# Optimization experiments

Hardware: AMD Instinct MI355X
Metric: run time of the kernel (lower is better)

## Reference

```python
import jax, jax.numpy as jnp
import numpy as np

# ---- fixed structural constants from the module source ----
BODY_PARTS = [[1, 2, 3], [4, 5, 6], [0, 7, 8, 9, 10], [11, 12, 13], [14, 15, 16]]
PART_EDGES = [[0, 2], [1, 2], [2, 3], [2, 4]]
N_JOINTS, N_PARTS = 17, 5
K_CHEB = 3  # ChebConv K=2 -> K+1 = 3 polynomial terms


def _pool_scatter_mats():
    # P[p, j] = 1/len(part_p) for j in part_p  (AdaptiveAvgPool1d(1) == mean)
    P = np.zeros((N_PARTS, N_JOINTS), np.float32)
    # S[j, p] = 1 if joint j belongs to part p (broadcast scatter)
    S = np.zeros((N_JOINTS, N_PARTS), np.float32)
    for p, idxs in enumerate(BODY_PARTS):
        for j in idxs:
            P[p, j] = 1.0 / len(idxs)
            S[j, p] = 1.0
    return jnp.asarray(P), jnp.asarray(S)


def _part_adj():
    # adj_mx_from_edges: symmetrize, add self loops, row-normalize
    A = np.zeros((N_PARTS, N_PARTS), np.float32)
    for i, j in PART_EDGES:
        A[i, j] = 1.0
    A = A + A.T  # edges are one-directional and disjoint -> symmetrize
    A = A + np.eye(N_PARTS, dtype=np.float32)
    A = A / A.sum(axis=1, keepdims=True)  # row-normalize
    return jnp.asarray(A)


def _cheb_basis(adj):
    # get_laplacian(normalize=True): L = I - D^{-1/2} A D^{-1/2}
    d_isqrt = jnp.sum(adj, axis=-1) ** (-0.5)
    L = jnp.eye(N_PARTS, dtype=adj.dtype) - (d_isqrt[:, None] * adj) * d_isqrt[None, :]
    I = jnp.eye(N_PARTS, dtype=adj.dtype)
    T2 = 2.0 * (L @ L) - I  # Chebyshev recurrence, K=2
    return jnp.stack([I, L, T2], axis=0)  # [3, 5, 5]


def setup_inputs() -> dict:
    key = jax.random.key(0)
    k1, k2 = jax.random.split(key)
    B, D = 8192, 512
    x = jax.random.normal(k1, (B, N_JOINTS, D), dtype=jnp.float32)
    # xavier-normal-like init for ChebConv weight [K+1, 1, in_c, out_c]
    scale = (2.0 / (D + D)) ** 0.5
    weight = jax.random.normal(k2, (K_CHEB, 1, D, D), dtype=jnp.float32) * scale
    bias = jnp.zeros((1, 1, D), dtype=jnp.float32)
    return {"x": x, "weight": weight, "bias": bias}


def reference(x, weight, bias):
    # x: [B, 17, D]; weight: [3, 1, D, D]; bias: [1, 1, D]
    P, S = _pool_scatter_mats()
    cheb = _cheb_basis(_part_adj())            # [3, 5, 5]
    part_feats = jnp.einsum('pj,bjd->bpd', P, x)              # part-wise mean pool
    prop = jnp.einsum('knm,bmd->kbnd', cheb, part_feats)      # Cheb propagation
    part_out = jnp.einsum('kbnd,kde->bne', prop, weight[:, 0]) + bias[0]  # [B, 5, D]
    return jnp.einsum('jp,bpd->bjd', S, part_out)             # broadcast to 17 joints
```

## Files before the change

### kernel.cpp

```cpp
#include <hip/hip_runtime.h>
#include <hip/hip_bf16.h>
#include <stdint.h>
#include <stddef.h>

typedef __attribute__((ext_vector_type(8))) short short8;
typedef __attribute__((ext_vector_type(4))) float f32x4;
typedef __attribute__((ext_vector_type(4))) unsigned int u32x4;

#define DIM   512
#define NJ    17
#define NPART 5
#define NB    8192
#define KDIM  1536
#define QROWS (NB*NPART)
#define ROWB  (KDIM*2)

struct Cheb { float c[3][5][5]; };

__device__ __forceinline__ void gload_lds16(const void* g, void* l) {
  __builtin_amdgcn_global_load_lds((__attribute__((address_space(1))) void*)(g),
                                   (__attribute__((address_space(3))) void*)(l),
                                   16, 0, 0);
}

__global__ __launch_bounds__(256) void pool_cheb_kernel(
    const float* __restrict__ x, __hip_bfloat16* __restrict__ Q, Cheb cb) {
  int gid = blockIdx.x * 256 + threadIdx.x;
  int b  = gid >> 7;
  int c4 = gid & 127;
  const float* xb = x + (size_t)b * (NJ * DIM) + (c4 << 2);

  f32x4 pf[5];
#pragma unroll
  for (int p = 0; p < 5; ++p) pf[p] = (f32x4){0.f, 0.f, 0.f, 0.f};

  constexpr int jpart[NJ] = {2,0,0,0,1,1,1,2,2,2,2,3,3,3,4,4,4};
#pragma unroll
  for (int j = 0; j < NJ; ++j) {
    f32x4 a = __builtin_nontemporal_load(
        reinterpret_cast<const f32x4*>(xb + j * DIM));
    pf[jpart[j]] += a;
  }
  constexpr float scl[5] = {1.f/3.f, 1.f/3.f, 0.2f, 1.f/3.f, 1.f/3.f};
#pragma unroll
  for (int p = 0; p < 5; ++p) pf[p] *= scl[p];

  char* qb = reinterpret_cast<char*>(Q);
  int cj = c4 >> 1;
#pragma unroll
  for (int k = 0; k < 3; ++k) {
#pragma unroll
    for (int n = 0; n < 5; ++n) {
      int row = b * 5 + n;
      f32x4 s = cb.c[k][n][0] * pf[0] + cb.c[k][n][1] * pf[1] +
                cb.c[k][n][2] * pf[2] + cb.c[k][n][3] * pf[3] +
                cb.c[k][n][4] * pf[4];
      alignas(8) __hip_bfloat16 o[4];
#pragma unroll
      for (int i = 0; i < 4; ++i) o[i] = __float2bfloat16(s[i]);
      int swc = (cj & 7) ^ (row & 7);
      size_t off = (size_t)row * ROWB + (size_t)(k * 8 + (cj >> 3)) * 128 +
                   (size_t)swc * 16 + (size_t)(c4 & 1) * 8;
      *reinterpret_cast<ushort4*>(qb + off) = *reinterpret_cast<const ushort4*>(o);
    }
  }
}

__global__ __launch_bounds__(256) void wt_kernel(
    const float* __restrict__ w, __hip_bfloat16* __restrict__ Wt) {
  int gid = blockIdx.x * 256 + threadIdx.x;
  int e = gid & 511;
  int chunk = gid >> 9;
  int kidx0 = chunk << 3;
  alignas(16) __hip_bfloat16 o[8];
#pragma unroll
  for (int i = 0; i < 8; ++i)
    o[i] = __float2bfloat16(w[(size_t)(kidx0 + i) * DIM + e]);
  int blk = kidx0 >> 6;
  int swc = ((kidx0 >> 3) & 7) ^ (e & 7);
  size_t off = (size_t)e * ROWB + (size_t)blk * 128 + (size_t)swc * 16;
  *reinterpret_cast<u32x4*>(reinterpret_cast<char*>(Wt) + off) =
      *reinterpret_cast<const u32x4*>(o);
}

__global__ __launch_bounds__(512, 2) void gemm_big_kernel(
    const __hip_bfloat16* __restrict__ Q, const __hip_bfloat16* __restrict__ Wt,
    const float* __restrict__ bias, float* __restrict__ out) {
  extern __shared__ __align__(16) char LDSbuf[];
  char* As0 = LDSbuf;
  char* As1 = LDSbuf + 40960;
  char* Bs0 = LDSbuf + 81920;
  char* Bs1 = LDSbuf + 114688;

  int tid  = threadIdx.x;
  int lane = tid & 63;
  int wave = tid >> 6;
  int wr = wave >> 1, wc = wave & 1;
  int m0 = blockIdx.y * 320;
  int n0 = blockIdx.x * 256;

  f32x4 acc[5][8] = {};

  const char* qb = reinterpret_cast<const char*>(Q);
  const char* wb = reinterpret_cast<const char*>(Wt);
  int sr8 = lane >> 3;
  int sc  = (lane & 7) * 16;

  const char* abase = qb + (size_t)(m0 + wave * 40 + sr8) * ROWB + sc;
  const char* bbase = wb + (size_t)(n0 + wave * 32 + sr8) * ROWB + sc;
  char* aldsw = (char*)0 + wave * 5120;
  char* bldsw = (char*)0 + wave * 4096;

  auto stage = [&](char* Abuf, char* Bbuf, int ks) {
#pragma unroll
    for (int i = 0; i < 5; ++i)
      gload_lds16(abase + (size_t)i * (8 * ROWB) + (size_t)ks * 128,
                  Abuf + (size_t)(aldsw - (char*)0) + i * 1024);
#pragma unroll
    for (int i = 0; i < 4; ++i)
      gload_lds16(bbase + (size_t)i * (8 * ROWB) + (size_t)ks * 128,
                  Bbuf + (size_t)(bldsw - (char*)0) + i * 1024);
  };

  auto compute = [&](const char* Abuf, const char* Bbuf) {
#pragma unroll
    for (int kk = 0; kk < 2; ++kk) {
      short8 af[5];
#pragma unroll
      for (int mi = 0; mi < 5; ++mi) {
        int r = wr * 80 + mi * 16 + (lane & 15);
        int c7 = (kk * 4 + (lane >> 4)) ^ (r & 7);
        af[mi] = *reinterpret_cast<const short8*>(Abuf + r * 128 + c7 * 16);
      }
#pragma unroll
      for (int h = 0; h < 2; ++h) {
        short8 bf[4];
#pragma unroll
        for (int nj = 0; nj < 4; ++nj) {
          int r = wc * 128 + (h * 4 + nj) * 16 + (lane & 15);
          int c7 = (kk * 4 + (lane >> 4)) ^ (r & 7);
          bf[nj] = *reinterpret_cast<const short8*>(Bbuf + r * 128 + c7 * 16);
        }
#pragma unroll
        for (int mi = 0; mi < 5; ++mi)
#pragma unroll
          for (int nj = 0; nj < 4; ++nj)
            acc[mi][h * 4 + nj] = __builtin_amdgcn_mfma_f32_16x16x32_bf16(
                af[mi], bf[nj], acc[mi][h * 4 + nj], 0, 0, 0);
      }
    }
  };

  stage(As0, Bs0, 0);
  __syncthreads();
  for (int ks = 0; ks < 22; ks += 2) {
    stage(As1, Bs1, ks + 1);
    compute(As0, Bs0);
    __syncthreads();
    stage(As0, Bs0, ks + 2);
    compute(As1, Bs1);
    __syncthreads();
  }
  stage(As1, Bs1, 23);
  compute(As0, Bs0);
  __syncthreads();
  compute(As1, Bs1);
  __syncthreads();

  float bs[8];
#pragma unroll
  for (int ni = 0; ni < 8; ++ni)
    bs[ni] = bias[n0 + wc * 128 + ni * 16 + (lane & 15)];

  char* eb = LDSbuf + wave * 8448;
  int halfsel = lane >> 5;
  int col4 = lane & 31;

#pragma unroll
  for (int mi = 0; mi < 5; ++mi) {
#pragma unroll
    for (int ni = 0; ni < 8; ++ni)
#pragma unroll
      for (int j = 0; j < 4; ++j) {
        int row = (lane >> 4) * 4 + j;
        *reinterpret_cast<float*>(
            eb + ((row * 132 + ni * 16 + (lane & 15)) << 2)) =
            acc[mi][ni][j] + bs[ni];
      }
#pragma unroll
    for (int rr = 0; rr < 8; ++rr) {
      int row = rr * 2 + halfsel;
      u32x4 v4 = *reinterpret_cast<const u32x4*>(
          eb + ((row * 132 + col4 * 4) << 2));
      int R = m0 + wr * 80 + mi * 16 + row;
      unsigned bb = (unsigned)R / 5u;
      int n = R - (int)bb * 5;
      unsigned mask = (n == 0) ? 0x0000Eu :
                      (n == 1) ? 0x00070u :
                      (n == 2) ? 0x00781u :
                      (n == 3) ? 0x03800u : 0x1C000u;
      float* op = out + (size_t)bb * (NJ * DIM) + (n0 + wc * 128 + col4 * 4);
      while (mask) {
        int jn = __builtin_ctz(mask);
        mask &= mask - 1;
        __builtin_nontemporal_store(v4, reinterpret_cast<u32x4*>(op + jn * DIM));
      }
    }
  }
}

__global__ __launch_bounds__(512) void gemm_scatter_kernel(
    const __hip_bfloat16* __restrict__ Q, const __hip_bfloat16* __restrict__ Wt,
    const float* __restrict__ bias, float* __restrict__ out) {
  __shared__ __align__(16) char LDSbuf[49152];
  char* As = LDSbuf;
  char* Bs = LDSbuf + 32768;

  int tid  = threadIdx.x;
  int lane = tid & 63;
  int wave = tid >> 6;
  int wr = wave >> 1, wc = wave & 1;
  int m0 = blockIdx.y * 256;
  int n0 = blockIdx.x * 128;

  f32x4 acc[4][4] = {};

  const char* qb = reinterpret_cast<const char*>(Q);
  const char* wb = reinterpret_cast<const char*>(Wt);
  int sr8 = lane >> 3;
  int sc  = (lane & 7) * 16;

  for (int ks = 0; ks < 24; ++ks) {
#pragma unroll
    for (int i = 0; i < 4; ++i) {
      int rbase = i * 64 + wave * 8;
      gload_lds16(qb + (size_t)(m0 + rbase + sr8) * ROWB + (size_t)ks * 128 + sc,
                  As + rbase * 128);
    }
#pragma unroll
    for (int i = 0; i < 2; ++i) {
      int rbase = i * 64 + wave * 8;
      gload_lds16(wb + (size_t)(n0 + rbase + sr8) * ROWB + (size_t)ks * 128 + sc,
                  Bs + rbase * 128);
    }
    __syncthreads();
#pragma unroll
    for (int kk = 0; kk < 2; ++kk) {
      short8 af[4], bfr[4];
#pragma unroll
      for (int mi = 0; mi < 4; ++mi) {
        int r = wr * 64 + mi * 16 + (lane & 15);
        int c7 = (kk * 4 + (lane >> 4)) ^ (r & 7);
        af[mi] = *reinterpret_cast<const short8*>(As + r * 128 + c7 * 16);
      }
#pragma unroll
      for (int ni = 0; ni < 4; ++ni) {
        int r = wc * 64 + ni * 16 + (lane & 15);
        int c7 = (kk * 4 + (lane >> 4)) ^ (r & 7);
        bfr[ni] = *reinterpret_cast<const short8*>(Bs + r * 128 + c7 * 16);
      }
#pragma unroll
      for (int mi = 0; mi < 4; ++mi)
#pragma unroll
        for (int ni = 0; ni < 4; ++ni)
          acc[mi][ni] = __builtin_amdgcn_mfma_f32_16x16x32_bf16(
              af[mi], bfr[ni], acc[mi][ni], 0, 0, 0);
    }
    __syncthreads();
  }

  int colbase = n0 + wc * 64 + (lane & 15);
  float bs[4];
#pragma unroll
  for (int ni = 0; ni < 4; ++ni) bs[ni] = bias[colbase + ni * 16];

  char* eb = LDSbuf + wave * 4352;
  int g4 = lane >> 4;
  int cc = lane & 15;

#pragma unroll
  for (int mi = 0; mi < 4; ++mi) {
#pragma unroll
    for (int ni = 0; ni < 4; ++ni)
#pragma unroll
      for (int j = 0; j < 4; ++j)
        *reinterpret_cast<float*>(
            eb + (((g4 * 4 + j) * 68 + ni * 16 + cc) << 2)) =
            acc[mi][ni][j] + bs[ni];

#pragma unroll
    for (int t = 0; t < 4; ++t) {
      u32x4 v4 = *reinterpret_cast<const u32x4*>(
          eb + ((((t * 4 + g4) * 68) + cc * 4) << 2));
      int R4 = m0 + wr * 64 + mi * 16 + t * 4 + g4;
      unsigned bb = (unsigned)R4 / 5u;
      int n = R4 - (int)bb * 5;
      unsigned mask = (n == 0) ? 0x0000Eu :
                      (n == 1) ? 0x00070u :
                      (n == 2) ? 0x00781u :
                      (n == 3) ? 0x03800u : 0x1C000u;
      float* op = out + (size_t)bb * (NJ * DIM) + (n0 + wc * 64 + cc * 4);
      while (mask) {
        int jn = __builtin_ctz(mask);
        mask &= mask - 1;
        __builtin_nontemporal_store(v4, reinterpret_cast<u32x4*>(op + jn * DIM));
      }
    }
  }
}

extern "C" void kernel_launch(void* const* d_in, const int* in_sizes, int n_in,
                              void* d_out, int out_size, void* d_ws, size_t ws_size,
                              hipStream_t stream) {
  const float* x    = (const float*)d_in[0];
  const float* w    = (const float*)d_in[1];
  const float* bias = (const float*)d_in[2];
  float* out = (float*)d_out;

  __hip_bfloat16* Q  = (__hip_bfloat16*)d_ws;
  __hip_bfloat16* Wt = (__hip_bfloat16*)((char*)d_ws + (size_t)QROWS * ROWB);

  Cheb cb;
  {
    double A[5][5] = {};
    const int e0[4] = {0, 1, 2, 2}, e1[4] = {2, 2, 3, 4};
    for (int t = 0; t < 4; ++t) { A[e0[t]][e1[t]] = 1.0; A[e1[t]][e0[t]] = 1.0; }
    for (int i = 0; i < 5; ++i) A[i][i] += 1.0;
    for (int i = 0; i < 5; ++i) {
      double rs = 0; for (int j = 0; j < 5; ++j) rs += A[i][j];
      for (int j = 0; j < 5; ++j) A[i][j] /= rs;
    }
    double L[5][5], T2[5][5];
    for (int i = 0; i < 5; ++i)
      for (int j = 0; j < 5; ++j) L[i][j] = (i == j ? 1.0 : 0.0) - A[i][j];
    for (int i = 0; i < 5; ++i)
      for (int j = 0; j < 5; ++j) {
        double s = 0; for (int m = 0; m < 5; ++m) s += L[i][m] * L[m][j];
        T2[i][j] = 2.0 * s - (i == j ? 1.0 : 0.0);
      }
    for (int i = 0; i < 5; ++i)
      for (int j = 0; j < 5; ++j) {
        cb.c[0][i][j] = (float)(i == j ? 1.0 : 0.0);
        cb.c[1][i][j] = (float)L[i][j];
        cb.c[2][i][j] = (float)T2[i][j];
      }
  }

  pool_cheb_kernel<<<(NB * 128) / 256, 256, 0, stream>>>(x, Q, cb);
  wt_kernel<<<(DIM * (KDIM / 8)) / 256, 256, 0, stream>>>(w, Wt);

  const int DYN_LDS = 147456;
  hipError_t e = hipFuncSetAttribute(
      reinterpret_cast<const void*>(gemm_big_kernel),
      hipFuncAttributeMaxDynamicSharedMemorySize, DYN_LDS);
  if (e == hipSuccess) {
    gemm_big_kernel<<<dim3(DIM / 256, QROWS / 320), 512, DYN_LDS, stream>>>(
        Q, Wt, bias, out);
  } else {
    gemm_scatter_kernel<<<dim3(DIM / 128, QROWS / 256), 512, 0, stream>>>(
        Q, Wt, bias, out);
  }
}
```

Measured before the change: 172.7 us.

## Fuse pooling/Chebyshev propagation into GEMM, staging A operand in LDS

Adds a fused kernel in which each 1024-thread block pools 32 batch items, applies the Chebyshev mixing and writes the bf16 A operand directly into LDS. It then runs the MFMA GEMM over the full 512 output columns and scatters the results to the 17 joints. This removes the global round trip of the Q intermediate and one kernel launch. The weight is re-laid out so that K tiles interleave with the pooling chunks. The cost is a single wave of work per block, with x loads serialized against compute behind syncthreads and no double buffering of B.

```diff
diff --git a/kernel.cpp b/kernel.cpp
--- a/kernel.cpp
+++ b/kernel.cpp
@@ -5,6 +5,7 @@
 
 typedef __attribute__((ext_vector_type(8))) short short8;
 typedef __attribute__((ext_vector_type(4))) float f32x4;
+typedef __attribute__((ext_vector_type(2))) float f32x2;
 typedef __attribute__((ext_vector_type(4))) unsigned int u32x4;
 
 #define DIM   512
@@ -23,6 +24,162 @@
                                    16, 0, 0);
 }
 
+__global__ __launch_bounds__(1024, 4) void fused_kernel(
+    const float* __restrict__ x, const __hip_bfloat16* __restrict__ Wt2,
+    const float* __restrict__ bias, float* __restrict__ out, Cheb cb) {
+  extern __shared__ __align__(16) char LDS[];
+  char* Aseg = LDS;
+  char* Bs   = LDS + 61440;
+
+  int tid  = threadIdx.x;
+  int lane = tid & 63;
+  int wave = tid >> 6;
+  int wr = wave >> 3;
+  int wc = wave & 7;
+  int b0    = blockIdx.x * 32;
+  int prow0 = blockIdx.x * 160;
+
+  f32x4 acc[5][4] = {};
+
+  int bl = tid >> 5;
+  int dd = tid & 31;
+  const float* xb = x + (size_t)(b0 + bl) * (NJ * DIM) + (dd << 1);
+  constexpr int jpart[NJ] = {2,0,0,0,1,1,1,2,2,2,2,3,3,3,4,4,4};
+  constexpr float scl[5] = {1.f/3.f, 1.f/3.f, 0.2f, 1.f/3.f, 1.f/3.f};
+
+  const char* wb = reinterpret_cast<const char*>(Wt2);
+
+  for (int db = 0; db < 8; ++db) {
+    f32x2 pf[5];
+#pragma unroll
+    for (int p = 0; p < 5; ++p) pf[p] = (f32x2){0.f, 0.f};
+    const float* xd = xb + db * 64;
+#pragma unroll
+    for (int j = 0; j < NJ; ++j) {
+      f32x2 a = __builtin_nontemporal_load(
+          reinterpret_cast<const f32x2*>(xd + j * DIM));
+      pf[jpart[j]] += a;
+    }
+#pragma unroll
+    for (int p = 0; p < 5; ++p) pf[p] *= scl[p];
+
+#pragma unroll
+    for (int k = 0; k < 3; ++k) {
+#pragma unroll
+      for (int n = 0; n < 5; ++n) {
+        int row = bl * 5 + n;
+        f32x2 s = cb.c[k][n][0] * pf[0] + cb.c[k][n][1] * pf[1] +
+                  cb.c[k][n][2] * pf[2] + cb.c[k][n][3] * pf[3] +
+                  cb.c[k][n][4] * pf[4];
+        alignas(4) __hip_bfloat16 o2[2];
+        o2[0] = __float2bfloat16(s[0]);
+        o2[1] = __float2bfloat16(s[1]);
+        *reinterpret_cast<unsigned int*>(
+            Aseg + k * 20480 + row * 128 +
+            (((dd >> 2) ^ (row & 7)) << 4) + ((dd & 3) << 2)) =
+            *reinterpret_cast<const unsigned int*>(o2);
+      }
+    }
+
+#pragma unroll
+    for (int k = 0; k < 3; ++k) {
+      int ks = db * 3 + k;
+#pragma unroll
+      for (int i = 0; i < 4; ++i) {
+        int rbase = i * 128 + wave * 8;
+        gload_lds16(wb + (size_t)(rbase + (lane >> 3)) * ROWB +
+                        (size_t)ks * 128 + (lane & 7) * 16,
+                    Bs + rbase * 128);
+      }
+      __syncthreads();
+
+      const char* Ab = Aseg + k * 20480;
+#pragma unroll
+      for (int kk = 0; kk < 2; ++kk) {
+        short8 af[5], bf[4];
+#pragma unroll
+        for (int mi = 0; mi < 5; ++mi) {
+          int r = wr * 80 + mi * 16 + (lane & 15);
+          int c7 = (kk * 4 + (lane >> 4)) ^ (r & 7);
+          af[mi] = *reinterpret_cast<const short8*>(Ab + r * 128 + c7 * 16);
+        }
+#pragma unroll
+        for (int nj = 0; nj < 4; ++nj) {
+          int r = wc * 64 + nj * 16 + (lane & 15);
+          int c7 = (kk * 4 + (lane >> 4)) ^ (r & 7);
+          bf[nj] = *reinterpret_cast<const short8*>(Bs + r * 128 + c7 * 16);
+        }
+#pragma unroll
+        for (int mi = 0; mi < 5; ++mi)
+#pragma unroll
+          for (int nj = 0; nj < 4; ++nj)
+            acc[mi][nj] = __builtin_amdgcn_mfma_f32_16x16x32_bf16(
+                af[mi], bf[nj], acc[mi][nj], 0, 0, 0);
+      }
+      __syncthreads();
+    }
+  }
+
+  float bs[4];
+#pragma unroll
+  for (int ni = 0; ni < 4; ++ni)
+    bs[ni] = bias[wc * 64 + ni * 16 + (lane & 15)];
+
+  char* eb = LDS + wave * 4352;
+  int g4 = lane >> 4;
+  int cc = lane & 15;
+
+#pragma unroll
+  for (int mi = 0; mi < 5; ++mi) {
+#pragma unroll
+    for (int ni = 0; ni < 4; ++ni)
+#pragma unroll
+      for (int j = 0; j < 4; ++j)
+        *reinterpret_cast<float*>(
+            eb + (((g4 * 4 + j) * 68 + ni * 16 + cc) << 2)) =
+            acc[mi][ni][j] + bs[ni];
+
+#pragma unroll
+    for (int t = 0; t < 4; ++t) {
+      u32x4 v4 = *reinterpret_cast<const u32x4*>(
+          eb + ((((t * 4 + g4) * 68) + cc * 4) << 2));
+      int R = prow0 + wr * 80 + mi * 16 + t * 4 + g4;
+      unsigned bb = (unsigned)R / 5u;
+      int n = R - (int)bb * 5;
+      unsigned mask = (n == 0) ? 0x0000Eu :
+                      (n == 1) ? 0x00070u :
+                      (n == 2) ? 0x00781u :
+                      (n == 3) ? 0x03800u : 0x1C000u;
+      float* op = out + (size_t)bb * (NJ * DIM) + (wc * 64 + cc * 4);
+      while (mask) {
+        int jn = __builtin_ctz(mask);
+        mask &= mask - 1;
+        __builtin_nontemporal_store(v4, reinterpret_cast<u32x4*>(op + jn * DIM));
+      }
+    }
+  }
+}
+
+__global__ __launch_bounds__(256) void wt2_kernel(
+    const float* __restrict__ w, __hip_bfloat16* __restrict__ Wt2) {
+  int gid = blockIdx.x * 256 + threadIdx.x;
+  int e   = gid / 192;
+  int rem = gid - e * 192;
+  int ks  = rem >> 3;
+  int dg  = rem & 7;
+  int k   = ks % 3;
+  int db  = ks / 3;
+  alignas(16) __hip_bfloat16 o[8];
+#pragma unroll
+  for (int i = 0; i < 8; ++i)
+    o[i] = __float2bfloat16(
+        w[(size_t)k * (DIM * DIM) + (size_t)(db * 64 + dg * 8 + i) * DIM + e]);
+  size_t off = (size_t)e * ROWB + (size_t)ks * 128 +
+               (size_t)((dg ^ (e & 7)) << 4);
+  *reinterpret_cast<u32x4*>(reinterpret_cast<char*>(Wt2) + off) =
+      *reinterpret_cast<const u32x4*>(o);
+}
+
 __global__ __launch_bounds__(256) void pool_cheb_kernel(
     const float* __restrict__ x, __hip_bfloat16* __restrict__ Q, Cheb cb) {
   int gid = blockIdx.x * 256 + threadIdx.x;
@@ -33,7 +190,6 @@
   f32x4 pf[5];
 #pragma unroll
   for (int p = 0; p < 5; ++p) pf[p] = (f32x4){0.f, 0.f, 0.f, 0.f};
-
   constexpr int jpart[NJ] = {2,0,0,0,1,1,1,2,2,2,2,3,3,3,4,4,4};
 #pragma unroll
   for (int j = 0; j < NJ; ++j) {
@@ -108,18 +264,18 @@
 
   const char* abase = qb + (size_t)(m0 + wave * 40 + sr8) * ROWB + sc;
   const char* bbase = wb + (size_t)(n0 + wave * 32 + sr8) * ROWB + sc;
-  char* aldsw = (char*)0 + wave * 5120;
-  char* bldsw = (char*)0 + wave * 4096;
+  size_t aoff = wave * 5120;
+  size_t boff = wave * 4096;
 
   auto stage = [&](char* Abuf, char* Bbuf, int ks) {
 #pragma unroll
     for (int i = 0; i < 5; ++i)
       gload_lds16(abase + (size_t)i * (8 * ROWB) + (size_t)ks * 128,
-                  Abuf + (size_t)(aldsw - (char*)0) + i * 1024);
+                  Abuf + aoff + i * 1024);
 #pragma unroll
     for (int i = 0; i < 4; ++i)
       gload_lds16(bbase + (size_t)i * (8 * ROWB) + (size_t)ks * 128,
-                  Bbuf + (size_t)(bldsw - (char*)0) + i * 1024);
+                  Bbuf + boff + i * 1024);
   };
 
   auto compute = [&](const char* Abuf, const char* Bbuf) {
@@ -209,106 +365,6 @@
   }
 }
 
-__global__ __launch_bounds__(512) void gemm_scatter_kernel(
-    const __hip_bfloat16* __restrict__ Q, const __hip_bfloat16* __restrict__ Wt,
-    const float* __restrict__ bias, float* __restrict__ out) {
-  __shared__ __align__(16) char LDSbuf[49152];
-  char* As = LDSbuf;
-  char* Bs = LDSbuf + 32768;
-
-  int tid  = threadIdx.x;
-  int lane = tid & 63;
-  int wave = tid >> 6;
-  int wr = wave >> 1, wc = wave & 1;
-  int m0 = blockIdx.y * 256;
-  int n0 = blockIdx.x * 128;
-
-  f32x4 acc[4][4] = {};
-
-  const char* qb = reinterpret_cast<const char*>(Q);
-  const char* wb = reinterpret_cast<const char*>(Wt);
-  int sr8 = lane >> 3;
-  int sc  = (lane & 7) * 16;
-
-  for (int ks = 0; ks < 24; ++ks) {
-#pragma unroll
-    for (int i = 0; i < 4; ++i) {
-      int rbase = i * 64 + wave * 8;
-      gload_lds16(qb + (size_t)(m0 + rbase + sr8) * ROWB + (size_t)ks * 128 + sc,
-                  As + rbase * 128);
-    }
-#pragma unroll
-    for (int i = 0; i < 2; ++i) {
-      int rbase = i * 64 + wave * 8;
-      gload_lds16(wb + (size_t)(n0 + rbase + sr8) * ROWB + (size_t)ks * 128 + sc,
-                  Bs + rbase * 128);
-    }
-    __syncthreads();
-#pragma unroll
-    for (int kk = 0; kk < 2; ++kk) {
-      short8 af[4], bfr[4];
-#pragma unroll
-      for (int mi = 0; mi < 4; ++mi) {
-        int r = wr * 64 + mi * 16 + (lane & 15);
-        int c7 = (kk * 4 + (lane >> 4)) ^ (r & 7);
-        af[mi] = *reinterpret_cast<const short8*>(As + r * 128 + c7 * 16);
-      }
-#pragma unroll
-      for (int ni = 0; ni < 4; ++ni) {
-        int r = wc * 64 + ni * 16 + (lane & 15);
-        int c7 = (kk * 4 + (lane >> 4)) ^ (r & 7);
-        bfr[ni] = *reinterpret_cast<const short8*>(Bs + r * 128 + c7 * 16);
-      }
-#pragma unroll
-      for (int mi = 0; mi < 4; ++mi)
-#pragma unroll
-        for (int ni = 0; ni < 4; ++ni)
-          acc[mi][ni] = __builtin_amdgcn_mfma_f32_16x16x32_bf16(
-              af[mi], bfr[ni], acc[mi][ni], 0, 0, 0);
-    }
-    __syncthreads();
-  }
-
-  int colbase = n0 + wc * 64 + (lane & 15);
-  float bs[4];
-#pragma unroll
-  for (int ni = 0; ni < 4; ++ni) bs[ni] = bias[colbase + ni * 16];
-
-  char* eb = LDSbuf + wave * 4352;
-  int g4 = lane >> 4;
-  int cc = lane & 15;
-
-#pragma unroll
-  for (int mi = 0; mi < 4; ++mi) {
-#pragma unroll
-    for (int ni = 0; ni < 4; ++ni)
-#pragma unroll
-      for (int j = 0; j < 4; ++j)
-        *reinterpret_cast<float*>(
-            eb + (((g4 * 4 + j) * 68 + ni * 16 + cc) << 2)) =
-            acc[mi][ni][j] + bs[ni];
-
-#pragma unroll
-    for (int t = 0; t < 4; ++t) {
-      u32x4 v4 = *reinterpret_cast<const u32x4*>(
-          eb + ((((t * 4 + g4) * 68) + cc * 4) << 2));
-      int R4 = m0 + wr * 64 + mi * 16 + t * 4 + g4;
-      unsigned bb = (unsigned)R4 / 5u;
-      int n = R4 - (int)bb * 5;
-      unsigned mask = (n == 0) ? 0x0000Eu :
-                      (n == 1) ? 0x00070u :
-                      (n == 2) ? 0x00781u :
-                      (n == 3) ? 0x03800u : 0x1C000u;
-      float* op = out + (size_t)bb * (NJ * DIM) + (n0 + wc * 64 + cc * 4);
-      while (mask) {
-        int jn = __builtin_ctz(mask);
-        mask &= mask - 1;
-        __builtin_nontemporal_store(v4, reinterpret_cast<u32x4*>(op + jn * DIM));
-      }
-    }
-  }
-}
-
 extern "C" void kernel_launch(void* const* d_in, const int* in_sizes, int n_in,
                               void* d_out, int out_size, void* d_ws, size_t ws_size,
                               hipStream_t stream) {
@@ -317,8 +373,9 @@
   const float* bias = (const float*)d_in[2];
   float* out = (float*)d_out;
 
-  __hip_bfloat16* Q  = (__hip_bfloat16*)d_ws;
-  __hip_bfloat16* Wt = (__hip_bfloat16*)((char*)d_ws + (size_t)QROWS * ROWB);
+  __hip_bfloat16* Wt2 = (__hip_bfloat16*)d_ws;
+  __hip_bfloat16* Q   = (__hip_bfloat16*)((char*)d_ws + (2u << 20));
+  __hip_bfloat16* Wt  = (__hip_bfloat16*)((char*)d_ws + (128u << 20));
 
   Cheb cb;
   {
@@ -346,18 +403,23 @@
       }
   }
 
+  const int FUSED_LDS = 126976;
+  hipError_t e1 = hipFuncSetAttribute(
+      reinterpret_cast<const void*>(fused_kernel),
+      hipFuncAttributeMaxDynamicSharedMemorySize, FUSED_LDS);
+  if (e1 == hipSuccess) {
+    wt2_kernel<<<384, 256, 0, stream>>>(w, Wt2);
+    fused_kernel<<<NB / 32, 1024, FUSED_LDS, stream>>>(x, Wt2, bias, out, cb);
+    return;
+  }
+
   pool_cheb_kernel<<<(NB * 128) / 256, 256, 0, stream>>>(x, Q, cb);
   wt_kernel<<<(DIM * (KDIM / 8)) / 256, 256, 0, stream>>>(w, Wt);
-
   const int DYN_LDS = 147456;
-  hipError_t e = hipFuncSetAttribute(
+  hipError_t e2 = hipFuncSetAttribute(
       reinterpret_cast<const void*>(gemm_big_kernel),
       hipFuncAttributeMaxDynamicSharedMemorySize, DYN_LDS);
-  if (e == hipSuccess) {
-    gemm_big_kernel<<<dim3(DIM / 256, QROWS / 320), 512, DYN_LDS, stream>>>(
-        Q, Wt, bias, out);
-  } else {
-    gemm_scatter_kernel<<<dim3(DIM / 128, QROWS / 256), 512, 0, stream>>>(
-        Q, Wt, bias, out);
-  }
-}
+  (void)e2;
+  gemm_big_kernel<<<dim3(DIM / 256, QROWS / 320), 512, DYN_LDS, stream>>>(
+      Q, Wt, bias, out);
+}
```

Result: slower. 228.5 us (+32.3%).
